# Optimization experiments

Hardware: AMD Instinct MI355X
Metric: run time of the kernel (lower is better)

## Reference

```python
import jax, jax.numpy as jnp
import numpy as np


def _patches(x, k):
    """Replicate F.unfold(x[None,None], kernel_size=k, padding=k//2).
    x: [H, W] -> [k*k, H, W], zero-padded, row-major kernel order (kh, kw)."""
    H, W = x.shape
    p = k // 2
    xp = jnp.pad(x, p)
    return jnp.stack([xp[i:i + H, j:j + W] for i in range(k) for j in range(k)])


def setup_inputs() -> dict:
    key = jax.random.key(0)
    H, W = 1536, 2048
    predict_counting_map = jax.random.uniform(key, (1, 1, H, W), dtype=jnp.float32)
    return {"predict_counting_map": predict_counting_map, "loc_kernel_size": 3, "stride": 4}


def reference(predict_counting_map, loc_kernel_size, stride):
    k = loc_kernel_size
    center = (k * k) // 2
    threshold = 0.5
    m = jax.nn.relu(predict_counting_map[0, 0])            # [H, W] (interpolate scale 1 = identity)
    H, W = m.shape

    patches = _patches(m, k)                               # [k*k, H, W] == unfolded_map
    # local-max mask: argmax over window equals center tap (first-occurrence ties, like torch)
    unfolded_max_mask = (jnp.argmax(patches, axis=0) == center)
    # conv2d with ones kernel == windowed sum of the (zero-padded) patches
    predict_cnt = patches.sum(axis=0)
    predict_filter = (predict_cnt > threshold).astype(jnp.float32) * unfolded_max_mask

    # L1-normalized window weights (F.normalize p=1, eps=1e-12); patches are >= 0 post-relu
    denom = jnp.maximum(jnp.abs(patches).sum(axis=0), 1e-12)
    pred_coord_weight = patches / denom                    # [k*k, H, W]

    coord_h = jnp.broadcast_to(jnp.arange(H, dtype=jnp.float32)[:, None], (H, W))
    coord_w = jnp.broadcast_to(jnp.arange(W, dtype=jnp.float32)[None, :], (H, W))
    pred_coord_h = (_patches(coord_h, k) * pred_coord_weight).sum(axis=0)  # [H, W]
    pred_coord_w = (_patches(coord_w, k) * pred_coord_weight).sum(axis=0)

    # points = stride * coord + 0.5 at pixels where predict_filter is set;
    # returned as fixed-shape maps (filter mask + scaled centroid coords).
    s = jnp.float32(stride)
    out = jnp.stack([predict_filter,
                     s * pred_coord_w + 0.5,
                     s * pred_coord_h + 0.5])              # [3, H, W]
    return out
```

## Files before the change

### kernel.cpp

```cpp
#include <hip/hip_runtime.h>

constexpr int H = 1536;
constexpr int W = 2048;

__global__ __launch_bounds__(256)
void counting_post_kernel(const float* __restrict__ in,
                          const int* __restrict__ stride_p,
                          float* __restrict__ out) {
    const int W4 = W / 4;
    const int tid = blockIdx.x * blockDim.x + threadIdx.x;
    const int r  = tid / W4;
    const int c0 = (tid - r * W4) * 4;
    if (r >= H) return;

    const float s = (float)(*stride_p);

    float v[3][6];
#pragma unroll
    for (int dr = 0; dr < 3; ++dr) {
        const int rr = r + dr - 1;
        if (rr < 0 || rr >= H) {
#pragma unroll
            for (int j = 0; j < 6; ++j) v[dr][j] = 0.f;
        } else {
            const float* row = in + (size_t)rr * W + c0;
            const float4 mid = *reinterpret_cast<const float4*>(row);
            v[dr][1] = fmaxf(mid.x, 0.f);
            v[dr][2] = fmaxf(mid.y, 0.f);
            v[dr][3] = fmaxf(mid.z, 0.f);
            v[dr][4] = fmaxf(mid.w, 0.f);
            v[dr][0] = (c0 > 0)     ? fmaxf(row[-1], 0.f) : 0.f;
            v[dr][5] = (c0 + 4 < W) ? fmaxf(row[4],  0.f) : 0.f;
        }
    }

    float f_o[4], cw_o[4], ch_o[4];
#pragma unroll
    for (int p = 0; p < 4; ++p) {
        const float w00 = v[0][p], w01 = v[0][p+1], w02 = v[0][p+2];
        const float w10 = v[1][p], w11 = v[1][p+1], w12 = v[1][p+2];
        const float w20 = v[2][p], w21 = v[2][p+1], w22 = v[2][p+2];

        const float sum = w00 + w01 + w02 + w10 + w11 + w12 + w20 + w21 + w22;

        const bool mask = (w11 > w00) && (w11 > w01) && (w11 > w02) && (w11 > w10)
                       && (w11 >= w12) && (w11 >= w20) && (w11 >= w21) && (w11 >= w22);
        f_o[p] = (sum > 0.5f && mask) ? 1.f : 0.f;

        const float denom = fmaxf(sum, 1e-12f);
        const float inv   = 1.f / denom;

        const int c = c0 + p;
        const float wh = (float)(r - 1) * (w00 + w01 + w02)
                       + (float)(r    ) * (w10 + w11 + w12)
                       + (float)(r + 1) * (w20 + w21 + w22);
        const float ww = (float)(c - 1) * (w00 + w10 + w20)
                       + (float)(c    ) * (w01 + w11 + w21)
                       + (float)(c + 1) * (w02 + w12 + w22);

        cw_o[p] = s * (ww * inv) + 0.5f;
        ch_o[p] = s * (wh * inv) + 0.5f;
    }

    const size_t base  = (size_t)r * W + c0;
    const size_t plane = (size_t)H * W;
    *reinterpret_cast<float4*>(out + base)             = make_float4(f_o[0],  f_o[1],  f_o[2],  f_o[3]);
    *reinterpret_cast<float4*>(out + plane + base)     = make_float4(cw_o[0], cw_o[1], cw_o[2], cw_o[3]);
    *reinterpret_cast<float4*>(out + 2 * plane + base) = make_float4(ch_o[0], ch_o[1], ch_o[2], ch_o[3]);
}

extern "C" void kernel_launch(void* const* d_in, const int* in_sizes, int n_in,
                              void* d_out, int out_size, void* d_ws, size_t ws_size,
                              hipStream_t stream) {
    const float* in      = (const float*)d_in[0];
    const int*   stride  = (const int*)d_in[2];
    float*       out     = (float*)d_out;

    const int threads = 256;
    const int total   = H * (W / 4);
    const int blocks  = (total + threads - 1) / threads;
    counting_post_kernel<<<blocks, threads, 0, stream>>>(in, stride, out);
}
```

Before: 84.30 us.

## Process eight pixels per thread with shared column sums and nontemporal stores

Each thread now handles eight output pixels instead of four, which cuts halo reloads and index math per pixel. Column sums are computed once and reused for the window sum and the weighted coordinate sums. The weighted sums are rewritten algebraically as coord*sum plus an offset, and the division becomes a hardware reciprocal. Outputs are written with nontemporal stores to avoid polluting the cache. These changes trade a small precision change (approximate rcp, reassociated sums) and higher register use for less arithmetic and memory traffic.

```diff
diff --git a/kernel.cpp b/kernel.cpp
--- a/kernel.cpp
+++ b/kernel.cpp
@@ -2,82 +2,104 @@
 
 constexpr int H = 1536;
 constexpr int W = 2048;
+constexpr int W8 = W / 8;
+
+typedef float vf4 __attribute__((ext_vector_type(4)));
 
 __global__ __launch_bounds__(256)
 void counting_post_kernel(const float* __restrict__ in,
                           const int* __restrict__ stride_p,
                           float* __restrict__ out) {
-    const int W4 = W / 4;
     const int tid = blockIdx.x * blockDim.x + threadIdx.x;
-    const int r  = tid / W4;
-    const int c0 = (tid - r * W4) * 4;
-    if (r >= H) return;
+    const int r  = tid >> 8;
+    const int c0 = (tid & (W8 - 1)) << 3;
 
     const float s = (float)(*stride_p);
 
-    float v[3][6];
+    float v[3][10];
 #pragma unroll
     for (int dr = 0; dr < 3; ++dr) {
         const int rr = r + dr - 1;
         if (rr < 0 || rr >= H) {
 #pragma unroll
-            for (int j = 0; j < 6; ++j) v[dr][j] = 0.f;
+            for (int j = 0; j < 10; ++j) v[dr][j] = 0.f;
         } else {
             const float* row = in + (size_t)rr * W + c0;
-            const float4 mid = *reinterpret_cast<const float4*>(row);
-            v[dr][1] = fmaxf(mid.x, 0.f);
-            v[dr][2] = fmaxf(mid.y, 0.f);
-            v[dr][3] = fmaxf(mid.z, 0.f);
-            v[dr][4] = fmaxf(mid.w, 0.f);
+            const vf4 a = *reinterpret_cast<const vf4*>(row);
+            const vf4 b = *reinterpret_cast<const vf4*>(row + 4);
+            v[dr][1] = fmaxf(a.x, 0.f);
+            v[dr][2] = fmaxf(a.y, 0.f);
+            v[dr][3] = fmaxf(a.z, 0.f);
+            v[dr][4] = fmaxf(a.w, 0.f);
+            v[dr][5] = fmaxf(b.x, 0.f);
+            v[dr][6] = fmaxf(b.y, 0.f);
+            v[dr][7] = fmaxf(b.z, 0.f);
+            v[dr][8] = fmaxf(b.w, 0.f);
             v[dr][0] = (c0 > 0)     ? fmaxf(row[-1], 0.f) : 0.f;
-            v[dr][5] = (c0 + 4 < W) ? fmaxf(row[4],  0.f) : 0.f;
+            v[dr][9] = (c0 + 8 < W) ? fmaxf(row[8],  0.f) : 0.f;
         }
     }
 
-    float f_o[4], cw_o[4], ch_o[4];
+    float cs[10];
 #pragma unroll
-    for (int p = 0; p < 4; ++p) {
+    for (int j = 0; j < 10; ++j) cs[j] = (v[0][j] + v[1][j]) + v[2][j];
+
+    const float rf = (float)r;
+    const float cb = (float)c0;
+
+    float f_o[8], cw_o[8], ch_o[8];
+#pragma unroll
+    for (int p = 0; p < 8; ++p) {
         const float w00 = v[0][p], w01 = v[0][p+1], w02 = v[0][p+2];
         const float w10 = v[1][p], w11 = v[1][p+1], w12 = v[1][p+2];
         const float w20 = v[2][p], w21 = v[2][p+1], w22 = v[2][p+2];
 
-        const float sum = w00 + w01 + w02 + w10 + w11 + w12 + w20 + w21 + w22;
+        const float sum = (cs[p] + cs[p+1]) + cs[p+2];
 
-        const bool mask = (w11 > w00) && (w11 > w01) && (w11 > w02) && (w11 > w10)
-                       && (w11 >= w12) && (w11 >= w20) && (w11 >= w21) && (w11 >= w22);
+        const float emax = fmaxf(fmaxf(fmaxf(w00, w01), w02), w10);
+        const float lmax = fmaxf(fmaxf(fmaxf(w12, w20), w21), w22);
+        const bool mask = (w11 > emax) && (w11 >= lmax);
         f_o[p] = (sum > 0.5f && mask) ? 1.f : 0.f;
 
-        const float denom = fmaxf(sum, 1e-12f);
-        const float inv   = 1.f / denom;
+        const float inv = __builtin_amdgcn_rcpf(fmaxf(sum, 1e-12f));
 
-        const int c = c0 + p;
-        const float wh = (float)(r - 1) * (w00 + w01 + w02)
-                       + (float)(r    ) * (w10 + w11 + w12)
-                       + (float)(r + 1) * (w20 + w21 + w22);
-        const float ww = (float)(c - 1) * (w00 + w10 + w20)
-                       + (float)(c    ) * (w01 + w11 + w21)
-                       + (float)(c + 1) * (w02 + w12 + w22);
+        const float rs0 = (w00 + w01) + w02;
+        const float rs2 = (w20 + w21) + w22;
+        const float wh  = fmaf(rf,     sum, rs2 - rs0);
+        const float ww  = fmaf(cb + (float)p, sum, cs[p+2] - cs[p]);
 
-        cw_o[p] = s * (ww * inv) + 0.5f;
-        ch_o[p] = s * (wh * inv) + 0.5f;
+        cw_o[p] = fmaf(s, ww * inv, 0.5f);
+        ch_o[p] = fmaf(s, wh * inv, 0.5f);
     }
 
     const size_t base  = (size_t)r * W + c0;
     const size_t plane = (size_t)H * W;
-    *reinterpret_cast<float4*>(out + base)             = make_float4(f_o[0],  f_o[1],  f_o[2],  f_o[3]);
-    *reinterpret_cast<float4*>(out + plane + base)     = make_float4(cw_o[0], cw_o[1], cw_o[2], cw_o[3]);
-    *reinterpret_cast<float4*>(out + 2 * plane + base) = make_float4(ch_o[0], ch_o[1], ch_o[2], ch_o[3]);
+
+    vf4 o0 = {f_o[0],  f_o[1],  f_o[2],  f_o[3]};
+    vf4 o1 = {f_o[4],  f_o[5],  f_o[6],  f_o[7]};
+    __builtin_nontemporal_store(o0, reinterpret_cast<vf4*>(out + base));
+    __builtin_nontemporal_store(o1, reinterpret_cast<vf4*>(out + base + 4));
+
+    vf4 w0 = {cw_o[0], cw_o[1], cw_o[2], cw_o[3]};
+    vf4 w1 = {cw_o[4], cw_o[5], cw_o[6], cw_o[7]};
+    __builtin_nontemporal_store(w0, reinterpret_cast<vf4*>(out + plane + base));
+    __builtin_nontemporal_store(w1, reinterpret_cast<vf4*>(out + plane + base + 4));
+
+    vf4 h0 = {ch_o[0], ch_o[1], ch_o[2], ch_o[3]};
+    vf4 h1 = {ch_o[4], ch_o[5], ch_o[6], ch_o[7]};
+    __builtin_nontemporal_store(h0, reinterpret_cast<vf4*>(out + 2 * plane + base));
+    __builtin_nontemporal_store(h1, reinterpret_cast<vf4*>(out + 2 * plane + base + 4));
 }
 
 extern "C" void kernel_launch(void* const* d_in, const int* in_sizes, int n_in,
                               void* d_out, int out_size, void* d_ws, size_t ws_size,
                               hipStream_t stream) {
-    const float* in      = (const float*)d_in[0];
-    const int*   stride  = (const int*)d_in[2];
-    float*       out     = (float*)d_out;
+    const float* in     = (const float*)d_in[0];
+    const int*   stride = (const int*)d_in[2];
+    float*       out    = (float*)d_out;
 
     const int threads = 256;
-    const int total   = H * (W / 4);
-    const int blocks  = (total + threads - 1) / threads;
+    const int total   = H * W8;
+    const int blocks  = total / threads;
     counting_post_kernel<<<blocks, threads, 0, stream>>>(in, stride, out);
 }
```

Result: slower. 87.01 us (+3.2%).
